# Kernel tuning notes

Measured on AMD Instinct MI355X. Metric: run time of the kernel, lower is better.

## Reference

```python
import jax, jax.numpy as jnp
import numpy as np

RESOLUTION = 2048
NUM_BEAMS = 256
K0 = 50.0
TWO_PI = 2.0 * np.pi


def setup_inputs() -> dict:
    key = jax.random.key(0)
    ks = jax.random.split(key, 6)
    # meshgrid buffers (indexing='ij')
    x = jnp.linspace(-1.0, 1.0, RESOLUTION, dtype=jnp.float32)
    y = jnp.linspace(-1.0, 1.0, RESOLUTION, dtype=jnp.float32)
    X, Y = jnp.meshgrid(x, y, indexing='ij')
    return {
        'theta': jax.random.uniform(ks[0], (NUM_BEAMS,), jnp.float32) * TWO_PI,
        'real': jax.random.normal(ks[1], (NUM_BEAMS,), jnp.float32) * 0.1,
        'imag': jax.random.normal(ks[2], (NUM_BEAMS,), jnp.float32) * 0.1,
        'x0': jax.random.uniform(ks[3], (NUM_BEAMS,), jnp.float32) * 2.0 - 1.0,
        'y0': jax.random.uniform(ks[4], (NUM_BEAMS,), jnp.float32) * 2.0 - 1.0,
        'log_sigma': jnp.zeros((NUM_BEAMS,), jnp.float32),
        'X': X,
        'Y': Y,
    }


def reference(theta, real, imag, x0, y0, log_sigma, X, Y):
    # Accumulate E = sum_i coeff_i * exp(i*phase_i) * envelope_i over beams,
    # carrying (E_re, E_im) through a scan so only grid-sized buffers live at once.
    def body(carry, p):
        E_re, E_im = carry
        th, re, im, px, py, ls = p
        kx = K0 * jnp.cos(th)
        ky = K0 * jnp.sin(th)
        sigma = jnp.exp(ls) + 0.001
        env = jnp.exp(-((X - px) ** 2 + (Y - py) ** 2) / sigma ** 2)
        phase = kx * X + ky * Y
        c = jnp.cos(phase)
        s = jnp.sin(phase)
        # (re + i*im) * (c + i*s) * env
        E_re = E_re + env * (re * c - im * s)
        E_im = E_im + env * (re * s + im * c)
        return (E_re, E_im), None

    params = jnp.stack([theta, real, imag, x0, y0, log_sigma], axis=1)  # [B, 6]
    zero = jnp.zeros_like(X)
    (E_re, E_im), _ = jax.lax.scan(body, (zero, zero), params)
    return E_re ** 2 + E_im ** 2  # |E|^2
```

## Files before the change

kernel.cpp:

```cpp
#include <hip/hip_runtime.h>
#include <math.h>

#define RES 2048
#define NB  256

typedef _Float16 f16;
typedef __fp16   fp16x2 __attribute__((ext_vector_type(2)));
typedef _Float16 f16x8 __attribute__((ext_vector_type(8)));
typedef float    f32x16 __attribute__((ext_vector_type(16)));

#define BM 128
#define BN 128
#define BK 16
#define NKT (NB / BK)
#define PL  (BM * BK)

#define STEP (2.0f / 2047.0f)

__device__ __forceinline__ f16x8 neg8(f16x8 v) {
    union { f16x8 h; unsigned int u[4]; } x;
    x.h = v;
    #pragma unroll
    for (int i = 0; i < 4; ++i) x.u[i] ^= 0x80008000u;
    return x.h;
}

__device__ __forceinline__ unsigned int pk2(float lo, float hi) {
    union { fp16x2 h; unsigned int u; } x;
    x.h = __builtin_amdgcn_cvt_pkrtz(lo, hi);
    return x.u;
}

__device__ __forceinline__ int swzE(int row, int k) {
    return (row * BK + k) ^ ((row & 7) << 3);
}

__global__ __launch_bounds__(512) void ewald_fused(
    const float* __restrict__ theta, const float* __restrict__ reA,
    const float* __restrict__ imA, const float* __restrict__ x0A,
    const float* __restrict__ y0A, const float* __restrict__ lsA,
    const float* __restrict__ X, const float* __restrict__ Y,
    float* __restrict__ out)
{
    __shared__ f16 smA[2][2][PL];
    __shared__ f16 smB[2][2][PL];
    __shared__ float4 sP0[NB];
    __shared__ float4 sP1[NB];

    const int t    = threadIdx.x;
    const int lane = t & 63;
    const int wave = t >> 6;
    const int wm   = wave >> 2;
    const int wn   = wave & 3;
    const int la   = lane & 31;
    const int lg   = lane >> 5;

    const int flat = blockIdx.x;
    const int swz  = (flat & 7) * 32 + (flat >> 3);
    const int m0   = (swz >> 4) * BM;
    const int n0   = (swz & 15) * BN;

    if (t < NB) {
        const int b = t;
        const float th = theta[b];
        const float s = __sinf(th), c = __cosf(th);
        const float sig = __expf(lsA[b]) + 0.001f;
        sP0[b] = make_float4(50.0f * c, 50.0f * s, x0A[b], y0A[b]);
        sP1[b] = make_float4(reA[b], imA[b], 1.0f / (sig * sig), 0.0f);
    }
    __syncthreads();

    const int kk2  = (t & 7) * 2;
    const int grp  = t >> 3;
    const int row0 = grp * 2;

    const float xv0 = -1.0f + (float)(m0 + row0)     * STEP;
    const float xv1 = -1.0f + (float)(m0 + row0 + 1) * STEP;
    const float yv0 = -1.0f + (float)(n0 + row0)     * STEP;
    const float yv1 = -1.0f + (float)(n0 + row0 + 1) * STEP;

    const int e0 = swzE(row0, kk2);
    const int e1 = swzE(row0 + 1, kk2);

    #define EVAL(bf, kt)                                                      \
    do {                                                                      \
        const int b0_ = (kt) * BK + kk2;                                      \
        float aR_[2][2], aI_[2][2], bR_[2][2], bI_[2][2];                     \
        _Pragma("unroll")                                                     \
        for (int jb = 0; jb < 2; ++jb) {                                      \
            const float4 p0 = sP0[b0_ + jb];                                  \
            const float4 p1 = sP1[b0_ + jb];                                  \
            _Pragma("unroll")                                                 \
            for (int r = 0; r < 2; ++r) {                                     \
                const float xv = r ? xv1 : xv0;                               \
                const float phx = p0.x * xv;                                  \
                const float sx_ = __sinf(phx), cx_ = __cosf(phx);             \
                const float dx = xv - p0.z;                                   \
                const float ex = __expf(-dx * dx * p1.z);                     \
                aR_[jb][r] = ex * (p1.x * cx_ - p1.y * sx_);                  \
                aI_[jb][r] = ex * (p1.x * sx_ + p1.y * cx_);                  \
                const float yv = r ? yv1 : yv0;                               \
                const float phy = p0.y * yv;                                  \
                const float sy_ = __sinf(phy), cy_ = __cosf(phy);             \
                const float dy = yv - p0.w;                                   \
                const float ey = __expf(-dy * dy * p1.z);                     \
                bR_[jb][r] = ey * cy_;                                        \
                bI_[jb][r] = ey * sy_;                                        \
            }                                                                 \
        }                                                                     \
        _Pragma("unroll")                                                     \
        for (int r = 0; r < 2; ++r) {                                         \
            const int e_ = r ? e1 : e0;                                       \
            *(unsigned int*)&smA[bf][0][e_] = pk2(aR_[0][r], aR_[1][r]);      \
            *(unsigned int*)&smA[bf][1][e_] = pk2(aI_[0][r], aI_[1][r]);      \
            *(unsigned int*)&smB[bf][0][e_] = pk2(bR_[0][r], bR_[1][r]);      \
            *(unsigned int*)&smB[bf][1][e_] = pk2(bI_[0][r], bI_[1][r]);      \
        }                                                                     \
    } while (0)

    const int offA0 = swzE(wm * 64 +  0 + la, lg * 8);
    const int offA1 = swzE(wm * 64 + 32 + la, lg * 8);
    const int offB  = swzE(wn * 32 + la, lg * 8);

    f32x16 accRe0 = (f32x16)0.0f, accIm0 = (f32x16)0.0f;
    f32x16 accRe1 = (f32x16)0.0f, accIm1 = (f32x16)0.0f;

    EVAL(0, 0);
    __syncthreads();

    for (int kt = 0; kt < NKT; ++kt) {
        const int cur = kt & 1;
        const f16x8 aR0 = *(const f16x8*)&smA[cur][0][offA0];
        const f16x8 aR1 = *(const f16x8*)&smA[cur][0][offA1];
        const f16x8 aI0 = *(const f16x8*)&smA[cur][1][offA0];
        const f16x8 aI1 = *(const f16x8*)&smA[cur][1][offA1];
        const f16x8 bR  = *(const f16x8*)&smB[cur][0][offB];
        const f16x8 bI  = *(const f16x8*)&smB[cur][1][offB];
        const f16x8 bN  = neg8(bI);

        __builtin_amdgcn_s_setprio(1);
        accRe0 = __builtin_amdgcn_mfma_f32_32x32x16_f16(aR0, bR, accRe0, 0, 0, 0);
        accIm0 = __builtin_amdgcn_mfma_f32_32x32x16_f16(aR0, bI, accIm0, 0, 0, 0);
        accRe1 = __builtin_amdgcn_mfma_f32_32x32x16_f16(aR1, bR, accRe1, 0, 0, 0);
        accIm1 = __builtin_amdgcn_mfma_f32_32x32x16_f16(aR1, bI, accIm1, 0, 0, 0);
        accRe0 = __builtin_amdgcn_mfma_f32_32x32x16_f16(aI0, bN, accRe0, 0, 0, 0);
        accIm0 = __builtin_amdgcn_mfma_f32_32x32x16_f16(aI0, bR, accIm0, 0, 0, 0);
        accRe1 = __builtin_amdgcn_mfma_f32_32x32x16_f16(aI1, bN, accRe1, 0, 0, 0);
        accIm1 = __builtin_amdgcn_mfma_f32_32x32x16_f16(aI1, bR, accIm1, 0, 0, 0);
        __builtin_amdgcn_s_setprio(0);

        if (kt + 1 < NKT)
            EVAL(cur ^ 1, kt + 1);

        __syncthreads();
    }

    const int gn     = n0 + wn * 32 + la;
    const int gmBase = m0 + wm * 64;
    #pragma unroll
    for (int r = 0; r < 16; ++r) {
        const int row = (r & 3) + 8 * (r >> 2) + 4 * lg;
        const float er = accRe0[r], ei = accIm0[r];
        out[(size_t)(gmBase + row) * RES + gn] = er * er + ei * ei;
    }
    #pragma unroll
    for (int r = 0; r < 16; ++r) {
        const int row = (r & 3) + 8 * (r >> 2) + 4 * lg;
        const float er = accRe1[r], ei = accIm1[r];
        out[(size_t)(gmBase + 32 + row) * RES + gn] = er * er + ei * ei;
    }
    #undef EVAL
}

extern "C" void kernel_launch(void* const* d_in, const int* in_sizes, int n_in,
                              void* d_out, int out_size, void* d_ws, size_t ws_size,
                              hipStream_t stream) {
    const float* theta = (const float*)d_in[0];
    const float* reA   = (const float*)d_in[1];
    const float* imA   = (const float*)d_in[2];
    const float* x0A   = (const float*)d_in[3];
    const float* y0A   = (const float*)d_in[4];
    const float* lsA   = (const float*)d_in[5];
    const float* X     = (const float*)d_in[6];
    const float* Y     = (const float*)d_in[7];
    float* out = (float*)d_out;

    ewald_fused<<<256, 512, 0, stream>>>(theta, reA, imA, x0A, y0A, lsA,
                                         X, Y, out);
}
```

Baseline: 23.37 us.

## Generate factor tiles by complex recurrence across rows and double the K tile

The per-beam x and y factor tiles are now built with a multiplicative recurrence. Each thread computes sin/cos/exp once at a base row, then steps 16 rows at a time using a precomputed rotation (cos/sin of k·DD) and a Gaussian ratio that is itself updated geometrically. Per-beam step constants are precomputed into shared memory. The K tile doubles to 32, so there are half as many barriers and two MFMA sub-steps per tile, and the LDS swizzle is changed to match. The goal is to cut transcendental work in the evaluation phase, at the cost of more rounding error from the recurrence and more LDS use.

```diff
diff --git a/kernel.cpp b/kernel.cpp
--- a/kernel.cpp
+++ b/kernel.cpp
@@ -11,11 +11,12 @@
 
 #define BM 128
 #define BN 128
-#define BK 16
+#define BK 32
 #define NKT (NB / BK)
-#define PL  (BM * BK)
+#define PL32 (BM * BK)
 
 #define STEP (2.0f / 2047.0f)
+#define DD   (16.0f * STEP)
 
 __device__ __forceinline__ f16x8 neg8(f16x8 v) {
     union { f16x8 h; unsigned int u[4]; } x;
@@ -29,10 +30,6 @@
     union { fp16x2 h; unsigned int u; } x;
     x.h = __builtin_amdgcn_cvt_pkrtz(lo, hi);
     return x.u;
-}
-
-__device__ __forceinline__ int swzE(int row, int k) {
-    return (row * BK + k) ^ ((row & 7) << 3);
 }
 
 __global__ __launch_bounds__(512) void ewald_fused(
@@ -42,10 +39,12 @@
     const float* __restrict__ X, const float* __restrict__ Y,
     float* __restrict__ out)
 {
-    __shared__ f16 smA[2][2][PL];
-    __shared__ f16 smB[2][2][PL];
+    __shared__ f16 smA[2][2][PL32];
+    __shared__ f16 smB[2][2][PL32];
     __shared__ float4 sP0[NB];
     __shared__ float4 sP1[NB];
+    __shared__ float4 sP2[NB];
+    __shared__ float  sW[NB];
 
     const int t    = threadIdx.x;
     const int lane = t & 63;
@@ -64,63 +63,76 @@
         const int b = t;
         const float th = theta[b];
         const float s = __sinf(th), c = __cosf(th);
+        const float kx = 50.0f * c, ky = 50.0f * s;
         const float sig = __expf(lsA[b]) + 0.001f;
-        sP0[b] = make_float4(50.0f * c, 50.0f * s, x0A[b], y0A[b]);
-        sP1[b] = make_float4(reA[b], imA[b], 1.0f / (sig * sig), 0.0f);
+        const float is2 = 1.0f / (sig * sig);
+        sP0[b] = make_float4(kx, ky, x0A[b], y0A[b]);
+        sP1[b] = make_float4(reA[b], imA[b], is2, DD * is2);
+        sP2[b] = make_float4(__cosf(kx * DD), __sinf(kx * DD),
+                             __cosf(ky * DD), __sinf(ky * DD));
+        sW[b]  = __expf(-2.0f * DD * DD * is2);
     }
     __syncthreads();
 
-    const int kk2  = (t & 7) * 2;
-    const int grp  = t >> 3;
-    const int row0 = grp * 2;
-
-    const float xv0 = -1.0f + (float)(m0 + row0)     * STEP;
-    const float xv1 = -1.0f + (float)(m0 + row0 + 1) * STEP;
-    const float yv0 = -1.0f + (float)(n0 + row0)     * STEP;
-    const float yv1 = -1.0f + (float)(n0 + row0 + 1) * STEP;
-
-    const int e0 = swzE(row0, kk2);
-    const int e1 = swzE(row0 + 1, kk2);
+    const int side = t >> 8;
+    const int u    = t & 255;
+    const int bp   = u & 15;
+    const int rg   = u >> 4;
+    const float x0r = -1.0f + (float)((side ? n0 : m0) + rg) * STEP;
+    f16* const evBase = side ? &smB[0][0][0] : &smA[0][0][0];
+    const int e00 = rg * 32 + ((bp * 2) ^ ((rg & 3) << 3));
 
     #define EVAL(bf, kt)                                                      \
     do {                                                                      \
-        const int b0_ = (kt) * BK + kk2;                                      \
-        float aR_[2][2], aI_[2][2], bR_[2][2], bI_[2][2];                     \
+        float vRe[2], vIm[2], rho[2], cdv[2], sdv[2], wv[2];                  \
         _Pragma("unroll")                                                     \
         for (int jb = 0; jb < 2; ++jb) {                                      \
-            const float4 p0 = sP0[b0_ + jb];                                  \
-            const float4 p1 = sP1[b0_ + jb];                                  \
-            _Pragma("unroll")                                                 \
-            for (int r = 0; r < 2; ++r) {                                     \
-                const float xv = r ? xv1 : xv0;                               \
-                const float phx = p0.x * xv;                                  \
-                const float sx_ = __sinf(phx), cx_ = __cosf(phx);             \
-                const float dx = xv - p0.z;                                   \
-                const float ex = __expf(-dx * dx * p1.z);                     \
-                aR_[jb][r] = ex * (p1.x * cx_ - p1.y * sx_);                  \
-                aI_[jb][r] = ex * (p1.x * sx_ + p1.y * cx_);                  \
-                const float yv = r ? yv1 : yv0;                               \
-                const float phy = p0.y * yv;                                  \
-                const float sy_ = __sinf(phy), cy_ = __cosf(phy);             \
-                const float dy = yv - p0.w;                                   \
-                const float ey = __expf(-dy * dy * p1.z);                     \
-                bR_[jb][r] = ey * cy_;                                        \
-                bI_[jb][r] = ey * sy_;                                        \
+            const int b_ = (kt) * BK + bp * 2 + jb;                           \
+            const float4 p0 = sP0[b_];                                        \
+            const float4 p1 = sP1[b_];                                        \
+            const float4 p2 = sP2[b_];                                        \
+            const float k_ = side ? p0.y : p0.x;                              \
+            const float p_ = side ? p0.w : p0.z;                              \
+            cdv[jb] = side ? p2.z : p2.x;                                     \
+            sdv[jb] = side ? p2.w : p2.y;                                     \
+            wv[jb]  = sW[b_];                                                 \
+            const float phi = k_ * x0r;                                       \
+            const float sn = __sinf(phi), cs = __cosf(phi);                   \
+            const float dx = x0r - p_;                                        \
+            const float e0 = __expf(-dx * dx * p1.z);                         \
+            rho[jb] = __expf(-(2.0f * dx + DD) * p1.w);                       \
+            if (side) { vRe[jb] = e0 * cs; vIm[jb] = e0 * sn; }               \
+            else {                                                            \
+                vRe[jb] = e0 * (p1.x * cs - p1.y * sn);                       \
+                vIm[jb] = e0 * (p1.x * sn + p1.y * cs);                       \
             }                                                                 \
         }                                                                     \
+        const int eb = (bf) * 2 * PL32 + e00;                                 \
         _Pragma("unroll")                                                     \
-        for (int r = 0; r < 2; ++r) {                                         \
-            const int e_ = r ? e1 : e0;                                       \
-            *(unsigned int*)&smA[bf][0][e_] = pk2(aR_[0][r], aR_[1][r]);      \
-            *(unsigned int*)&smA[bf][1][e_] = pk2(aI_[0][r], aI_[1][r]);      \
-            *(unsigned int*)&smB[bf][0][e_] = pk2(bR_[0][r], bR_[1][r]);      \
-            *(unsigned int*)&smB[bf][1][e_] = pk2(bI_[0][r], bI_[1][r]);      \
+        for (int r = 0; r < 8; ++r) {                                         \
+            *(unsigned int*)&evBase[eb + r * 512]        = pk2(vRe[0], vRe[1]); \
+            *(unsigned int*)&evBase[eb + PL32 + r * 512] = pk2(vIm[0], vIm[1]); \
+            _Pragma("unroll")                                                 \
+            for (int jb = 0; jb < 2; ++jb) {                                  \
+                const float t1 = vRe[jb] * cdv[jb] - vIm[jb] * sdv[jb];       \
+                const float t2 = vRe[jb] * sdv[jb] + vIm[jb] * cdv[jb];       \
+                vRe[jb] = t1 * rho[jb];                                       \
+                vIm[jb] = t2 * rho[jb];                                       \
+                rho[jb] *= wv[jb];                                            \
+            }                                                                 \
         }                                                                     \
     } while (0)
 
-    const int offA0 = swzE(wm * 64 +  0 + la, lg * 8);
-    const int offA1 = swzE(wm * 64 + 32 + la, lg * 8);
-    const int offB  = swzE(wn * 32 + la, lg * 8);
+    const int xk = (la & 3) << 3;
+    int offA[2][2], offBf[2];
+    #pragma unroll
+    for (int ks = 0; ks < 2; ++ks) {
+        #pragma unroll
+        for (int sub = 0; sub < 2; ++sub)
+            offA[sub][ks] = (wm * 64 + sub * 32 + la) * 32
+                          + ((ks * 16 + lg * 8) ^ xk);
+        offBf[ks] = (wn * 32 + la) * 32 + ((ks * 16 + lg * 8) ^ xk);
+    }
 
     f32x16 accRe0 = (f32x16)0.0f, accIm0 = (f32x16)0.0f;
     f32x16 accRe1 = (f32x16)0.0f, accIm1 = (f32x16)0.0f;
@@ -130,23 +142,29 @@
 
     for (int kt = 0; kt < NKT; ++kt) {
         const int cur = kt & 1;
-        const f16x8 aR0 = *(const f16x8*)&smA[cur][0][offA0];
-        const f16x8 aR1 = *(const f16x8*)&smA[cur][0][offA1];
-        const f16x8 aI0 = *(const f16x8*)&smA[cur][1][offA0];
-        const f16x8 aI1 = *(const f16x8*)&smA[cur][1][offA1];
-        const f16x8 bR  = *(const f16x8*)&smB[cur][0][offB];
-        const f16x8 bI  = *(const f16x8*)&smB[cur][1][offB];
-        const f16x8 bN  = neg8(bI);
+        const f16* sA = &smA[0][0][0] + cur * 2 * PL32;
+        const f16* sB = &smB[0][0][0] + cur * 2 * PL32;
 
         __builtin_amdgcn_s_setprio(1);
-        accRe0 = __builtin_amdgcn_mfma_f32_32x32x16_f16(aR0, bR, accRe0, 0, 0, 0);
-        accIm0 = __builtin_amdgcn_mfma_f32_32x32x16_f16(aR0, bI, accIm0, 0, 0, 0);
-        accRe1 = __builtin_amdgcn_mfma_f32_32x32x16_f16(aR1, bR, accRe1, 0, 0, 0);
-        accIm1 = __builtin_amdgcn_mfma_f32_32x32x16_f16(aR1, bI, accIm1, 0, 0, 0);
-        accRe0 = __builtin_amdgcn_mfma_f32_32x32x16_f16(aI0, bN, accRe0, 0, 0, 0);
-        accIm0 = __builtin_amdgcn_mfma_f32_32x32x16_f16(aI0, bR, accIm0, 0, 0, 0);
-        accRe1 = __builtin_amdgcn_mfma_f32_32x32x16_f16(aI1, bN, accRe1, 0, 0, 0);
-        accIm1 = __builtin_amdgcn_mfma_f32_32x32x16_f16(aI1, bR, accIm1, 0, 0, 0);
+        #pragma unroll
+        for (int ks = 0; ks < 2; ++ks) {
+            const f16x8 aR0 = *(const f16x8*)&sA[offA[0][ks]];
+            const f16x8 aR1 = *(const f16x8*)&sA[offA[1][ks]];
+            const f16x8 aI0 = *(const f16x8*)&sA[PL32 + offA[0][ks]];
+            const f16x8 aI1 = *(const f16x8*)&sA[PL32 + offA[1][ks]];
+            const f16x8 bR  = *(const f16x8*)&sB[offBf[ks]];
+            const f16x8 bI  = *(const f16x8*)&sB[PL32 + offBf[ks]];
+            const f16x8 bN  = neg8(bI);
+
+            accRe0 = __builtin_amdgcn_mfma_f32_32x32x16_f16(aR0, bR, accRe0, 0, 0, 0);
+            accIm0 = __builtin_amdgcn_mfma_f32_32x32x16_f16(aR0, bI, accIm0, 0, 0, 0);
+            accRe1 = __builtin_amdgcn_mfma_f32_32x32x16_f16(aR1, bR, accRe1, 0, 0, 0);
+            accIm1 = __builtin_amdgcn_mfma_f32_32x32x16_f16(aR1, bI, accIm1, 0, 0, 0);
+            accRe0 = __builtin_amdgcn_mfma_f32_32x32x16_f16(aI0, bN, accRe0, 0, 0, 0);
+            accIm0 = __builtin_amdgcn_mfma_f32_32x32x16_f16(aI0, bR, accIm0, 0, 0, 0);
+            accRe1 = __builtin_amdgcn_mfma_f32_32x32x16_f16(aI1, bN, accRe1, 0, 0, 0);
+            accIm1 = __builtin_amdgcn_mfma_f32_32x32x16_f16(aI1, bR, accIm1, 0, 0, 0);
+        }
         __builtin_amdgcn_s_setprio(0);
 
         if (kt + 1 < NKT)
```

After: 22.90 us. -2.0%, faster.

## Double block to 1024 threads, split A/B factor evaluation across thread halves

Applied to the files above, without the earlier changes.

Launches 1024 threads per block (16 waves), so each wave owns one 32x32 output tile instead of two. The first half of the threads evaluates the x-side (A) factors and the second half the y-side (B) factors, which halves the transcendental work per thread. The aim is to spread the sin/cos/exp work and the MFMA work over more waves and raise per-CU latency hiding. The cost is a larger block, fewer registers available per thread, and a divergence-free select between sides.

```diff
diff --git a/kernel.cpp b/kernel.cpp
--- a/kernel.cpp
+++ b/kernel.cpp
@@ -35,7 +35,7 @@
     return (row * BK + k) ^ ((row & 7) << 3);
 }
 
-__global__ __launch_bounds__(512) void ewald_fused(
+__global__ __launch_bounds__(1024) void ewald_fused(
     const float* __restrict__ theta, const float* __restrict__ reA,
     const float* __restrict__ imA, const float* __restrict__ x0A,
     const float* __restrict__ y0A, const float* __restrict__ lsA,
@@ -70,83 +70,75 @@
     }
     __syncthreads();
 
-    const int kk2  = (t & 7) * 2;
-    const int grp  = t >> 3;
+    const int side = t >> 9;
+    const int u    = t & 511;
+    const int bp   = u & 7;
+    const int grp  = u >> 3;
     const int row0 = grp * 2;
+    const int kk2  = bp * 2;
 
-    const float xv0 = -1.0f + (float)(m0 + row0)     * STEP;
-    const float xv1 = -1.0f + (float)(m0 + row0 + 1) * STEP;
-    const float yv0 = -1.0f + (float)(n0 + row0)     * STEP;
-    const float yv1 = -1.0f + (float)(n0 + row0 + 1) * STEP;
+    const float c0 = -1.0f + (float)((side ? n0 : m0) + row0) * STEP;
+    const float c1 = c0 + STEP;
 
+    f16* const evBase = side ? &smB[0][0][0] : &smA[0][0][0];
     const int e0 = swzE(row0, kk2);
     const int e1 = swzE(row0 + 1, kk2);
 
     #define EVAL(bf, kt)                                                      \
     do {                                                                      \
         const int b0_ = (kt) * BK + kk2;                                      \
-        float aR_[2][2], aI_[2][2], bR_[2][2], bI_[2][2];                     \
+        float vR[2][2], vI[2][2];                            \
         _Pragma("unroll")                                                     \
         for (int jb = 0; jb < 2; ++jb) {                                      \
             const float4 p0 = sP0[b0_ + jb];                                  \
             const float4 p1 = sP1[b0_ + jb];                                  \
+            const float k_ = side ? p0.y : p0.x;                              \
+            const float p_ = side ? p0.w : p0.z;                              \
             _Pragma("unroll")                                                 \
             for (int r = 0; r < 2; ++r) {                                     \
-                const float xv = r ? xv1 : xv0;                               \
-                const float phx = p0.x * xv;                                  \
-                const float sx_ = __sinf(phx), cx_ = __cosf(phx);             \
-                const float dx = xv - p0.z;                                   \
-                const float ex = __expf(-dx * dx * p1.z);                     \
-                aR_[jb][r] = ex * (p1.x * cx_ - p1.y * sx_);                  \
-                aI_[jb][r] = ex * (p1.x * sx_ + p1.y * cx_);                  \
-                const float yv = r ? yv1 : yv0;                               \
-                const float phy = p0.y * yv;                                  \
-                const float sy_ = __sinf(phy), cy_ = __cosf(phy);             \
-                const float dy = yv - p0.w;                                   \
-                const float ey = __expf(-dy * dy * p1.z);                     \
-                bR_[jb][r] = ey * cy_;                                        \
-                bI_[jb][r] = ey * sy_;                                        \
+                const float cv = r ? c1 : c0;                                 \
+                const float ph = k_ * cv;                                     \
+                const float sn = __sinf(ph), cs = __cosf(ph);                 \
+                const float d_ = cv - p_;                                     \
+                const float e_ = __expf(-d_ * d_ * p1.z);                     \
+                if (side) { vR[jb][r] = e_ * cs; vI[jb][r] = e_ * sn; }       \
+                else {                                                        \
+                    vR[jb][r] = e_ * (p1.x * cs - p1.y * sn);                 \
+                    vI[jb][r] = e_ * (p1.x * sn + p1.y * cs);                 \
+                }                                                             \
             }                                                                 \
         }                                                                     \
+        const int eb = (bf) * 2 * PL;                                         \
         _Pragma("unroll")                                                     \
         for (int r = 0; r < 2; ++r) {                                         \
-            const int e_ = r ? e1 : e0;                                       \
-            *(unsigned int*)&smA[bf][0][e_] = pk2(aR_[0][r], aR_[1][r]);      \
-            *(unsigned int*)&smA[bf][1][e_] = pk2(aI_[0][r], aI_[1][r]);      \
-            *(unsigned int*)&smB[bf][0][e_] = pk2(bR_[0][r], bR_[1][r]);      \
-            *(unsigned int*)&smB[bf][1][e_] = pk2(bI_[0][r], bI_[1][r]);      \
+            const int ee = (r ? e1 : e0) + eb;                                \
+            *(unsigned int*)&evBase[ee]      = pk2(vR[0][r], vR[1][r]);       \
+            *(unsigned int*)&evBase[ee + PL] = pk2(vI[0][r], vI[1][r]);       \
         }                                                                     \
     } while (0)
 
-    const int offA0 = swzE(wm * 64 +  0 + la, lg * 8);
-    const int offA1 = swzE(wm * 64 + 32 + la, lg * 8);
-    const int offB  = swzE(wn * 32 + la, lg * 8);
+    const int offA = swzE(wm * 32 + la, lg * 8);
+    const int offB = swzE(wn * 32 + la, lg * 8);
 
-    f32x16 accRe0 = (f32x16)0.0f, accIm0 = (f32x16)0.0f;
-    f32x16 accRe1 = (f32x16)0.0f, accIm1 = (f32x16)0.0f;
+    f32x16 accRe = (f32x16)0.0f, accIm = (f32x16)0.0f;
 
     EVAL(0, 0);
     __syncthreads();
 
     for (int kt = 0; kt < NKT; ++kt) {
         const int cur = kt & 1;
-        const f16x8 aR0 = *(const f16x8*)&smA[cur][0][offA0];
-        const f16x8 aR1 = *(const f16x8*)&smA[cur][0][offA1];
-        const f16x8 aI0 = *(const f16x8*)&smA[cur][1][offA0];
-        const f16x8 aI1 = *(const f16x8*)&smA[cur][1][offA1];
-        const f16x8 bR  = *(const f16x8*)&smB[cur][0][offB];
-        const f16x8 bI  = *(const f16x8*)&smB[cur][1][offB];
-        const f16x8 bN  = neg8(bI);
+        const int cb  = cur * 2 * PL;
+        const f16x8 aR = *(const f16x8*)&(&smA[0][0][0])[cb + offA];
+        const f16x8 aI = *(const f16x8*)&(&smA[0][0][0])[cb + PL + offA];
+        const f16x8 bR = *(const f16x8*)&(&smB[0][0][0])[cb + offB];
+        const f16x8 bI = *(const f16x8*)&(&smB[0][0][0])[cb + PL + offB];
+        const f16x8 bN = neg8(bI);
 
         __builtin_amdgcn_s_setprio(1);
-        accRe0 = __builtin_amdgcn_mfma_f32_32x32x16_f16(aR0, bR, accRe0, 0, 0, 0);
-        accIm0 = __builtin_amdgcn_mfma_f32_32x32x16_f16(aR0, bI, accIm0, 0, 0, 0);
-        accRe1 = __builtin_amdgcn_mfma_f32_32x32x16_f16(aR1, bR, accRe1, 0, 0, 0);
-        accIm1 = __builtin_amdgcn_mfma_f32_32x32x16_f16(aR1, bI, accIm1, 0, 0, 0);
-        accRe0 = __builtin_amdgcn_mfma_f32_32x32x16_f16(aI0, bN, accRe0, 0, 0, 0);
-        accIm0 = __builtin_amdgcn_mfma_f32_32x32x16_f16(aI0, bR, accIm0, 0, 0, 0);
-        accRe1 = __builtin_amdgcn_mfma_f32_32x32x16_f16(aI1, bN, accRe1, 0, 0, 0);
-        accIm1 = __builtin_amdgcn_mfma_f32_32x32x16_f16(aI1, bR, accIm1, 0, 0, 0);
+        accRe = __builtin_amdgcn_mfma_f32_32x32x16_f16(aR, bR, accRe, 0, 0, 0);
+        accIm = __builtin_amdgcn_mfma_f32_32x32x16_f16(aR, bI, accIm, 0, 0, 0);
+        accRe = __builtin_amdgcn_mfma_f32_32x32x16_f16(aI, bN, accRe, 0, 0, 0);
+        accIm = __builtin_amdgcn_mfma_f32_32x32x16_f16(aI, bR, accIm, 0, 0, 0);
         __builtin_amdgcn_s_setprio(0);
 
         if (kt + 1 < NKT)
@@ -156,18 +148,12 @@
     }
 
     const int gn     = n0 + wn * 32 + la;
-    const int gmBase = m0 + wm * 64;
+    const int gmBase = m0 + wm * 32;
     #pragma unroll
     for (int r = 0; r < 16; ++r) {
         const int row = (r & 3) + 8 * (r >> 2) + 4 * lg;
-        const float er = accRe0[r], ei = accIm0[r];
+        const float er = accRe[r], ei = accIm[r];
         out[(size_t)(gmBase + row) * RES + gn] = er * er + ei * ei;
-    }
-    #pragma unroll
-    for (int r = 0; r < 16; ++r) {
-        const int row = (r & 3) + 8 * (r >> 2) + 4 * lg;
-        const float er = accRe1[r], ei = accIm1[r];
-        out[(size_t)(gmBase + 32 + row) * RES + gn] = er * er + ei * ei;
     }
     #undef EVAL
 }
@@ -185,6 +171,6 @@
     const float* Y     = (const float*)d_in[7];
     float* out = (float*)d_out;
 
-    ewald_fused<<<256, 512, 0, stream>>>(theta, reA, imA, x0A, y0A, lsA,
-                                         X, Y, out);
+    ewald_fused<<<256, 1024, 0, stream>>>(theta, reA, imA, x0A, y0A, lsA,
+                                          X, Y, out);
 }
```

After: 24.37 us. 1.04x slower.
